# Kernel tuning notes

Measured on AMD Instinct MI355X. Metric: run time of the kernel, lower is better.

## Reference

```python
import jax, jax.numpy as jnp
import numpy as np

BANDLIMIT = 0.5
STEP_SCALE = 1.0  # refiner default step_scale_value
LN_EPS = 1e-5


def _layernorm(x, g, b):
    mu = jnp.mean(x, axis=-1, keepdims=True)
    xc = x - mu
    inv = jax.lax.rsqrt(jnp.mean(xc * xc, axis=-1, keepdims=True) + LN_EPS)
    return xc * inv * g + b


def setup_inputs() -> dict:
    key = jax.random.key(0)
    ks = jax.random.split(key, 12)
    B, C, H, W = 16, 384, 64, 64
    P = 192  # conj-sym half of state_dim=384
    x = jax.random.normal(ks[0], (B, C, H, W), dtype=jnp.float32)
    ln1_g = 1.0 + 0.1 * jax.random.normal(ks[1], (C,), dtype=jnp.float32)
    ln1_b = 0.1 * jax.random.normal(ks[2], (C,), dtype=jnp.float32)
    # stable diagonal A: negative real part, HiPPO-like imaginary ladder
    lam_re = -(0.3 + jax.random.uniform(ks[3], (P,), dtype=jnp.float32))
    lam_im = jnp.pi * jnp.arange(P, dtype=jnp.float32)
    Lambda = jnp.stack([lam_re, lam_im], axis=-1)          # [P,2] (re,im)
    Bmat = jax.random.normal(ks[4], (P, C, 2), dtype=jnp.float32) / np.sqrt(C)
    Cmat = jax.random.normal(ks[5], (C, P, 2), dtype=jnp.float32) / np.sqrt(P)
    D = jax.random.normal(ks[6], (C,), dtype=jnp.float32)
    log_step = jax.random.uniform(ks[7], (P,), dtype=jnp.float32,
                                  minval=float(np.log(1e-3)), maxval=float(np.log(0.1)))
    ln2_g = 1.0 + 0.1 * jax.random.normal(ks[8], (C,), dtype=jnp.float32)
    ln2_b = 0.1 * jax.random.normal(ks[9], (C,), dtype=jnp.float32)
    W_enc = jax.random.normal(ks[10], (2 * C, C), dtype=jnp.float32) / np.sqrt(C)
    W_dec = jax.random.normal(ks[11], (C, C), dtype=jnp.float32) / np.sqrt(C)
    return {"x": x, "ln1_g": ln1_g, "ln1_b": ln1_b, "Lambda": Lambda,
            "Bmat": Bmat, "Cmat": Cmat, "D": D, "log_step": log_step,
            "ln2_g": ln2_g, "ln2_b": ln2_b, "W_enc": W_enc, "W_dec": W_dec}


def reference(x, ln1_g, ln1_b, Lambda, Bmat, Cmat, D, log_step, ln2_g, ln2_b, W_enc, W_dec):
    Bsz, C, H, W = x.shape
    u = x.reshape(Bsz, C, H * W).transpose(0, 2, 1)        # [B, L, C]

    # --- S5Block: attn branch ---
    fx = _layernorm(u, ln1_g, ln1_b)
    res = fx

    lam = Lambda[..., 0] + 1j * Lambda[..., 1]             # [P] complex
    Bc = Bmat[..., 0] + 1j * Bmat[..., 1]                  # [P, C]
    Cc = Cmat[..., 0] + 1j * Cmat[..., 1]                  # [C, P]
    step = STEP_SCALE * jnp.exp(log_step)                  # [P]
    # bandlimit mask on C (as in S5 with bandlimit=0.5)
    freqs = (step / STEP_SCALE) * jnp.abs(Lambda[..., 1]) / (2.0 * jnp.pi)
    mask = (freqs < BANDLIMIT * 0.5).astype(Cc.dtype)
    Cc = Cc * mask
    # ZOH discretization
    lam_bar = jnp.exp(lam * step)                          # [P]
    B_bar = ((lam_bar - 1.0) / lam)[:, None] * Bc          # [P, C]
    Bu = jnp.einsum('ph,blh->blp', B_bar, fx.astype(B_bar.dtype))  # [B,L,P] complex
    lam_el = jnp.broadcast_to(lam_bar, Bu.shape)

    def binop(a, b):
        # linear recurrence composition: x <- a2*(a1*x + b1) + b2
        return a[0] * b[0], b[0] * a[1] + b[1]

    _, xs = jax.lax.associative_scan(binop, (lam_el, Bu), axis=1)  # [B,L,P]
    y = 2.0 * jnp.real(jnp.einsum('hp,blp->blh', Cc, xs)) + D * fx
    y = jax.nn.gelu(y, approximate=False) + res

    # --- S5Block: GEGLU FFN branch ---
    fy = _layernorm(y, ln2_g, ln2_b)
    z = fy @ W_enc.T                                       # [B,L,2C]
    z1, z2 = jnp.split(z, 2, axis=-1)
    z = z1 * jax.nn.gelu(z2, approximate=False)
    y = z @ W_dec.T + fy

    return y.transpose(0, 2, 1).reshape(Bsz, C, H, W)
```

## Files before the change

kernel.cpp:

```cpp
#include <hip/hip_runtime.h>
#include <hip/hip_bf16.h>
#include <math.h>

typedef __attribute__((ext_vector_type(4))) float f32x4;
typedef __attribute__((ext_vector_type(8))) short s16x8;
typedef unsigned short u16;
typedef unsigned int u32;

#define CDIM 384
#define PDIM 192
#define LDIM 4096
#define BSZ  16
#define MDIM 65536
#define KD   384
#define BM 128
#define BN 128
#define BK 32
#define NT (KD / BK)
#define BUFE (BM * BK)

__device__ __forceinline__ u16 f2bf(float f) {
    u32 x = __float_as_uint(f);
    x += 0x7fffu + ((x >> 16) & 1u);
    return (u16)(x >> 16);
}
__device__ __forceinline__ float bf2f(u16 v) {
    return __uint_as_float(((u32)v) << 16);
}
__device__ __forceinline__ float gelu_exact(float x) {
    return 0.5f * x * (1.0f + erff(x * 0.7071067811865476f));
}
__device__ __forceinline__ float gelu_fast(float x) {
    float w = -1.5957691216f * x * (1.0f + 0.044715f * x * x);
    return x / (1.0f + __expf(w));
}
__device__ __forceinline__ void gld_lds16(const u16* g, u16* l) {
    __builtin_amdgcn_global_load_lds(
        (const __attribute__((address_space(1))) void*)g,
        (__attribute__((address_space(3))) void*)l, 16, 0, 0);
}

__device__ __forceinline__ void swz_decode(int NY, int& mt, int& nt) {
    int bid = blockIdx.x + gridDim.x * blockIdx.y;
    int nwg = gridDim.x * gridDim.y;
    int cpx = nwg >> 3;
    int work = (bid & 7) * cpx + (bid >> 3);
    mt = work / NY;
    nt = work - mt * NY;
}

__global__ __launch_bounds__(256) void k_setup(
    const float* __restrict__ Lambda, const float* __restrict__ Bmat,
    const float* __restrict__ Cmat, const float* __restrict__ log_step,
    const float* __restrict__ W_enc, const float* __restrict__ W_dec,
    u16* __restrict__ Wb, u16* __restrict__ Wc, u16* __restrict__ We,
    u16* __restrict__ Wd, float* __restrict__ lam_bar)
{
    int idx = blockIdx.x * 256 + threadIdx.x;
    if (idx < 73728) {
        int p = idx / CDIM, c = idx % CDIM;
        float st  = expf(log_step[p]);
        float lre = Lambda[2*p], lim = Lambda[2*p+1];
        float el  = expf(lre * st);
        float lbr = el * cosf(lim * st);
        float lbi = el * sinf(lim * st);
        float dd  = lre*lre + lim*lim;
        float a = lbr - 1.0f, b = lbi;
        float cr = (a * lre + b * lim) / dd;
        float ci = (b * lre - a * lim) / dd;
        float Br = Bmat[2*(p*CDIM + c)], Bi = Bmat[2*(p*CDIM + c) + 1];
        Wb[p*KD + c]          = f2bf(cr*Br - ci*Bi);
        Wb[(PDIM + p)*KD + c] = f2bf(cr*Bi + ci*Br);
    } else if (idx < 147456) {
        int e = idx - 73728;
        int h = e / PDIM, p = e % PDIM;
        float st  = expf(log_step[p]);
        float lim = Lambda[2*p+1];
        float freq = st * fabsf(lim) / 6.283185307179586f;
        float sc = (freq < 0.25f) ? 2.0f : 0.0f;
        Wc[h*KD + p]        = f2bf( sc * Cmat[2*(h*PDIM + p)]);
        Wc[h*KD + PDIM + p] = f2bf(-sc * Cmat[2*(h*PDIM + p) + 1]);
    } else if (idx < 442368) {
        int e = idx - 147456;
        We[e] = f2bf(W_enc[e]);
    } else if (idx < 589824) {
        int e = idx - 442368;
        Wd[e] = f2bf(W_dec[e]);
    } else if (idx < 590016) {
        int p = idx - 589824;
        float st  = expf(log_step[p]);
        float lre = Lambda[2*p], lim = Lambda[2*p+1];
        float el  = expf(lre * st);
        lam_bar[2*p]   = el * cosf(lim * st);
        lam_bar[2*p+1] = el * sinf(lim * st);
    }
}

__global__ __launch_bounds__(256) void k_ln1(
    const float* __restrict__ x, const float* __restrict__ g,
    const float* __restrict__ bb, u16* __restrict__ fx)
{
    __shared__ float tile[CDIM * 36];
    __shared__ float mu_sh[32], inv_sh[32];
    int b  = blockIdx.x >> 7;
    int l0 = (blockIdx.x & 127) * 32;
    int tid = threadIdx.x;
    const float* src = x + ((size_t)b * CDIM) * LDIM + l0;
    #pragma unroll
    for (int it = 0; it < 12; it++) {
        int s = it * 256 + tid;
        int ch = s >> 3, c4 = (s & 7) * 4;
        float4 v = *(const float4*)(src + (size_t)ch * LDIM + c4);
        *(float4*)(tile + ch * 36 + c4) = v;
    }
    __syncthreads();
    int j = tid >> 3, k = tid & 7;
    float sum = 0.f, sq = 0.f;
    for (int c = k; c < CDIM; c += 8) {
        float v = tile[c * 36 + j];
        sum += v; sq += v * v;
    }
    sum += __shfl_xor(sum, 1); sq += __shfl_xor(sq, 1);
    sum += __shfl_xor(sum, 2); sq += __shfl_xor(sq, 2);
    sum += __shfl_xor(sum, 4); sq += __shfl_xor(sq, 4);
    float mu  = sum * (1.0f / CDIM);
    float var = sq * (1.0f / CDIM) - mu * mu;
    float inv = rsqrtf(var + 1e-5f);
    if (k == 0) { mu_sh[j] = mu; inv_sh[j] = inv; }
    __syncthreads();
    u16* dst = fx + ((size_t)(b * LDIM + l0)) * CDIM;
    #pragma unroll
    for (int it = 0; it < 12; it++) {
        int s  = it * 256 + tid;
        int cq = s % 96, jj = s / 96;
        int c  = cq * 4;
        float m2 = mu_sh[jj], iv = inv_sh[jj];
        float4 gv = *(const float4*)(g + c);
        float4 bv = *(const float4*)(bb + c);
        ushort4 o;
        o.x = f2bf((tile[(c+0)*36 + jj] - m2) * iv * gv.x + bv.x);
        o.y = f2bf((tile[(c+1)*36 + jj] - m2) * iv * gv.y + bv.y);
        o.z = f2bf((tile[(c+2)*36 + jj] - m2) * iv * gv.z + bv.z);
        o.w = f2bf((tile[(c+3)*36 + jj] - m2) * iv * gv.w + bv.w);
        *(ushort4*)(dst + (size_t)jj * CDIM + c) = o;
    }
}

template<bool SWAP>
__device__ __forceinline__ void gemm_core(
    const u16* __restrict__ A, int lda, const u16* __restrict__ Bw,
    int m0, int n0, u16* a_sh, u16* b_sh, f32x4 acc[4][4])
{
    const int tid  = threadIdx.x;
    const int w    = tid >> 6, lane = tid & 63;
    const int t16  = lane & 15, quad = lane >> 4;
    const int wm   = w >> 1,   wn   = w & 1;
    const int lr  = lane >> 2;
    const int cbg = (lane & 3) ^ ((lane >> 3) & 3);
    const u16* gA0 = A  + (size_t)(m0 + w*32 + lr) * lda + cbg*8;
    const u16* gA1 = gA0 + (size_t)16 * lda;
    const u16* gB0 = Bw + (size_t)(n0 + w*32 + lr) * KD + cbg*8;
    const u16* gB1 = gB0 + (size_t)16 * KD;
    u16* lA0 = a_sh + (w*32) * BK;
    u16* lA1 = lA0 + 16*BK;
    u16* lB0 = b_sh + (w*32) * BK;
    u16* lB1 = lB0 + 16*BK;
    const int pos = (quad ^ ((t16 >> 1) & 3)) * 8;
    const u16* ard = a_sh + (wm*64 + t16) * BK + pos;
    const u16* brd = b_sh + (wn*64 + t16) * BK + pos;
    #pragma unroll
    for (int i = 0; i < 4; i++)
        #pragma unroll
        for (int j = 0; j < 4; j++) acc[i][j] = (f32x4){0.f,0.f,0.f,0.f};
    gld_lds16(gA0, lA0);
    gld_lds16(gA1, lA1);
    gld_lds16(gB0, lB0);
    gld_lds16(gB1, lB1);
    gld_lds16(gA0 + BK, lA0 + BUFE);
    gld_lds16(gA1 + BK, lA1 + BUFE);
    gld_lds16(gB0 + BK, lB0 + BUFE);
    gld_lds16(gB1 + BK, lB1 + BUFE);
    #pragma unroll
    for (int t = 0; t < NT; ++t) {
        if (t < NT - 1) asm volatile("s_waitcnt vmcnt(4)" ::: "memory");
        else            asm volatile("s_waitcnt vmcnt(0)" ::: "memory");
        __builtin_amdgcn_s_barrier();
        __builtin_amdgcn_sched_barrier(0);
        if (t + 2 < NT) {
            const int kb = (t + 2) * BK;
            const int bo = ((t + 2) % 3) * BUFE;
            gld_lds16(gA0 + kb, lA0 + bo);
            gld_lds16(gA1 + kb, lA1 + bo);
            gld_lds16(gB0 + kb, lB0 + bo);
            gld_lds16(gB1 + kb, lB1 + bo);
        }
        __builtin_amdgcn_sched_barrier(0);
        const u16* ac = ard + (t % 3) * BUFE;
        const u16* bc = brd + (t % 3) * BUFE;
        s16x8 af[4], bfr[4];
        #pragma unroll
        for (int i = 0; i < 4; i++) af[i]  = *(const s16x8*)(ac + i*16*BK);
        #pragma unroll
        for (int j = 0; j < 4; j++) bfr[j] = *(const s16x8*)(bc + j*16*BK);
        #pragma unroll
        for (int i = 0; i < 4; i++)
            #pragma unroll
            for (int j = 0; j < 4; j++) {
                if (SWAP)
                    acc[i][j] = __builtin_amdgcn_mfma_f32_16x16x32_bf16(bfr[j], af[i], acc[i][j], 0,0,0);
                else
                    acc[i][j] = __builtin_amdgcn_mfma_f32_16x16x32_bf16(af[i], bfr[j], acc[i][j], 0,0,0);
            }
    }
}

__global__ __launch_bounds__(256) void k_gemm_bu(
    const u16* __restrict__ fx, const u16* __restrict__ Wb, u16* __restrict__ Bu)
{
    __shared__ __align__(16) u16 a_sh[3*BUFE], b_sh[3*BUFE];
    int mt, nt;
    swz_decode(gridDim.y, mt, nt);
    int m0 = mt * BM, n0 = nt * BN;
    f32x4 acc[4][4];
    gemm_core<false>(fx, CDIM, Wb, m0, n0, a_sh, b_sh, acc);
    int lane = threadIdx.x & 63, w = threadIdx.x >> 6;
    int t16 = lane & 15, quad = lane >> 4, wm = w >> 1, wn = w & 1;
    #pragma unroll
    for (int i = 0; i < 4; i++)
        #pragma unroll
        for (int j = 0; j < 4; j++)
            #pragma unroll
            for (int rr = 0; rr < 4; rr++) {
                int m = m0 + wm*64 + i*16 + quad*4 + rr;
                int n = n0 + wn*64 + j*16 + t16;
                Bu[(size_t)m * CDIM + n] = f2bf(acc[i][j][rr]);
            }
}

__global__ __launch_bounds__(256) void k_gemm_y(
    const u16* __restrict__ xs, const u16* __restrict__ Wc,
    const u16* __restrict__ fx, const float* __restrict__ Dv, u16* __restrict__ y)
{
    __shared__ __align__(16) u16 a_sh[3*BUFE], b_sh[3*BUFE];
    int mt, nt;
    swz_decode(gridDim.y, mt, nt);
    int m0 = mt * BM, n0 = nt * BN;
    f32x4 acc[4][4];
    gemm_core<false>(xs, CDIM, Wc, m0, n0, a_sh, b_sh, acc);
    int lane = threadIdx.x & 63, w = threadIdx.x >> 6;
    int t16 = lane & 15, quad = lane >> 4, wm = w >> 1, wn = w & 1;
    float dv[4];
    #pragma unroll
    for (int j = 0; j < 4; j++) dv[j] = Dv[n0 + wn*64 + j*16 + t16];
    #pragma unroll
    for (int i = 0; i < 4; i++)
        #pragma unroll
        for (int j = 0; j < 4; j++)
            #pragma unroll
            for (int rr = 0; rr < 4; rr++) {
                int m = m0 + wm*64 + i*16 + quad*4 + rr;
                int n = n0 + wn*64 + j*16 + t16;
                float fxv = bf2f(fx[(size_t)m * CDIM + n]);
                float v = acc[i][j][rr] + dv[j] * fxv;
                y[(size_t)m * CDIM + n] = f2bf(gelu_fast(v) + fxv);
            }
}

__global__ __launch_bounds__(256) void k_gemm_zg(
    const u16* __restrict__ fy, const u16* __restrict__ We, u16* __restrict__ zg)
{
    __shared__ __align__(16) u16 sh[6*BUFE];
    u16* a_sh = sh;
    u16* b_sh = sh + 3*BUFE;
    const int tid = threadIdx.x;
    const int w = tid >> 6, lane = tid & 63;
    const int t16 = lane & 15, quad = lane >> 4;
    const int wm = w >> 1, wn = w & 1;
    int mt, nt;
    swz_decode(gridDim.y, mt, nt);
    const int m0 = mt * BM;
    const int c0 = nt * 64;
    const int lr  = lane >> 2;
    const int cbg = (lane & 3) ^ ((lane >> 3) & 3);
    const u16* gA0 = fy + (size_t)(m0 + w*32 + lr) * CDIM + cbg*8;
    const u16* gA1 = gA0 + (size_t)16 * CDIM;
    int brow = c0 + w*32 + ((w >= 2) ? 320 : 0);
    const u16* gB0 = We + (size_t)(brow + lr) * KD + cbg*8;
    const u16* gB1 = gB0 + (size_t)16 * KD;
    u16* lA0 = a_sh + (w*32) * BK;
    u16* lA1 = lA0 + 16*BK;
    u16* lB0 = b_sh + (w*32) * BK;
    u16* lB1 = lB0 + 16*BK;
    const int pos = (quad ^ ((t16 >> 1) & 3)) * 8;
    const u16* ard = a_sh + (wm*64 + t16) * BK + pos;
    const u16* brd = b_sh + (wn*64 + t16) * BK + pos;
    f32x4 acc[4][4];
    #pragma unroll
    for (int i = 0; i < 4; i++)
        #pragma unroll
        for (int j = 0; j < 4; j++) acc[i][j] = (f32x4){0.f,0.f,0.f,0.f};
    gld_lds16(gA0, lA0);
    gld_lds16(gA1, lA1);
    gld_lds16(gB0, lB0);
    gld_lds16(gB1, lB1);
    gld_lds16(gA0 + BK, lA0 + BUFE);
    gld_lds16(gA1 + BK, lA1 + BUFE);
    gld_lds16(gB0 + BK, lB0 + BUFE);
    gld_lds16(gB1 + BK, lB1 + BUFE);
    #pragma unroll
    for (int t = 0; t < NT; ++t) {
        if (t < NT - 1) asm volatile("s_waitcnt vmcnt(4)" ::: "memory");
        else            asm volatile("s_waitcnt vmcnt(0)" ::: "memory");
        __builtin_amdgcn_s_barrier();
        __builtin_amdgcn_sched_barrier(0);
        if (t + 2 < NT) {
            const int kb = (t + 2) * BK;
            const int bo = ((t + 2) % 3) * BUFE;
            gld_lds16(gA0 + kb, lA0 + bo);
            gld_lds16(gA1 + kb, lA1 + bo);
            gld_lds16(gB0 + kb, lB0 + bo);
            gld_lds16(gB1 + kb, lB1 + bo);
        }
        __builtin_amdgcn_sched_barrier(0);
        const u16* ac = ard + (t % 3) * BUFE;
        const u16* bc = brd + (t % 3) * BUFE;
        s16x8 af[4], bfr[4];
        #pragma unroll
        for (int i = 0; i < 4; i++) af[i]  = *(const s16x8*)(ac + i*16*BK);
        #pragma unroll
        for (int j = 0; j < 4; j++) bfr[j] = *(const s16x8*)(brd ? (bc + j*16*BK) : nullptr);
        #pragma unroll
        for (int i = 0; i < 4; i++)
            #pragma unroll
            for (int j = 0; j < 4; j++)
                acc[i][j] = __builtin_amdgcn_mfma_f32_16x16x32_bf16(af[i], bfr[j], acc[i][j], 0,0,0);
    }
    __syncthreads();
    if (wn == 1) {
        #pragma unroll
        for (int i = 0; i < 4; i++)
            #pragma unroll
            for (int j = 0; j < 4; j++)
                #pragma unroll
                for (int rr = 0; rr < 4; rr++) {
                    int m = wm*64 + i*16 + quad*4 + rr;
                    int c = j*16 + t16;
                    sh[m*66 + c] = f2bf(gelu_fast(acc[i][j][rr]));
                }
    }
    __syncthreads();
    if (wn == 0) {
        #pragma unroll
        for (int i = 0; i < 4; i++)
            #pragma unroll
            for (int j = 0; j < 4; j++)
                #pragma unroll
                for (int rr = 0; rr < 4; rr++) {
                    int m = wm*64 + i*16 + quad*4 + rr;
                    int c = j*16 + t16;
                    float gv = bf2f(sh[m*66 + c]);
                    zg[(size_t)(m0 + m) * CDIM + c0 + c] = f2bf(acc[i][j][rr] * gv);
                }
    }
}

__global__ __launch_bounds__(256) void k_gemm_out(
    const u16* __restrict__ zg, const u16* __restrict__ Wd,
    const u16* __restrict__ fy, float* __restrict__ out)
{
    __shared__ __align__(16) u16 a_sh[3*BUFE], b_sh[3*BUFE];
    int mt, nt;
    swz_decode(gridDim.y, mt, nt);
    int m0 = mt * BM, n0 = nt * BN;
    f32x4 acc[4][4];
    gemm_core<true>(zg, CDIM, Wd, m0, n0, a_sh, b_sh, acc);
    int lane = threadIdx.x & 63, w = threadIdx.x >> 6;
    int t16 = lane & 15, quad = lane >> 4, wm = w >> 1, wn = w & 1;
    int b = m0 >> 12;
    #pragma unroll
    for (int i = 0; i < 4; i++)
        #pragma unroll
        for (int j = 0; j < 4; j++)
            #pragma unroll
            for (int rr = 0; rr < 4; rr++) {
                int nn = n0 + wn*64 + j*16 + quad*4 + rr;
                int mm = m0 + wm*64 + i*16 + t16;
                float fyv = bf2f(fy[(size_t)mm * CDIM + nn]);
                int l = mm & 4095;
                out[((size_t)(b * CDIM + nn)) * LDIM + l] = acc[i][j][rr] + fyv;
            }
}

__global__ __launch_bounds__(192) void k_scan_a(
    const u16* __restrict__ Bu, const float* __restrict__ lam_bar,
    float* __restrict__ summ)
{
    int b = blockIdx.x >> 6, ch = blockIdx.x & 63;
    int p = threadIdx.x;
    float lr = lam_bar[2*p], li = lam_bar[2*p+1];
    float xr = 0.f, xi = 0.f;
    const u16* base = Bu + (size_t)(b * LDIM + ch * 64) * CDIM;
    #pragma unroll 8
    for (int i = 0; i < 64; i++) {
        float br = bf2f(base[(size_t)i * CDIM + p]);
        float bi = bf2f(base[(size_t)i * CDIM + PDIM + p]);
        float nr = lr * xr - li * xi + br;
        float ni = lr * xi + li * xr + bi;
        xr = nr; xi = ni;
    }
    size_t o = (size_t)(b * 64 + ch) * CDIM + p;
    summ[o] = xr;
    summ[o + PDIM] = xi;
}

__global__ __launch_bounds__(256) void k_scan_b(
    const float* __restrict__ lam_bar, float* __restrict__ summ)
{
    int id = blockIdx.x * 256 + threadIdx.x;
    if (id >= BSZ * PDIM) return;
    int b = id / PDIM, p = id % PDIM;
    float ar = lam_bar[2*p], ai = lam_bar[2*p+1];
    #pragma unroll
    for (int s = 0; s < 6; s++) {
        float nr = ar * ar - ai * ai, ni = 2.f * ar * ai;
        ar = nr; ai = ni;
    }
    float cr = 0.f, ci = 0.f;
    #pragma unroll 4
    for (int ch = 0; ch < 64; ch++) {
        size_t o = (size_t)(b * 64 + ch) * CDIM + p;
        float sr = summ[o], si = summ[o + PDIM];
        summ[o] = cr; summ[o + PDIM] = ci;
        float nr = ar * cr - ai * ci + sr;
        float ni = ar * ci + ai * cr + si;
        cr = nr; ci = ni;
    }
}

__global__ __launch_bounds__(192) void k_scan_c(
    u16* __restrict__ Bu, const float* __restrict__ lam_bar,
    const float* __restrict__ summ)
{
    int b = blockIdx.x >> 6, ch = blockIdx.x & 63;
    int p = threadIdx.x;
    float lr = lam_bar[2*p], li = lam_bar[2*p+1];
    size_t oc = (size_t)(b * 64 + ch) * CDIM + p;
    float xr = summ[oc], xi = summ[oc + PDIM];
    u16* base = Bu + (size_t)(b * LDIM + ch * 64) * CDIM;
    #pragma unroll 8
    for (int i = 0; i < 64; i++) {
        float br = bf2f(base[(size_t)i * CDIM + p]);
        float bi = bf2f(base[(size_t)i * CDIM + PDIM + p]);
        float nr = lr * xr - li * xi + br;
        float ni = lr * xi + li * xr + bi;
        xr = nr; xi = ni;
        base[(size_t)i * CDIM + p] = f2bf(xr);
        base[(size_t)i * CDIM + PDIM + p] = f2bf(xi);
    }
}

__global__ __launch_bounds__(256) void k_ln2(
    const u16* __restrict__ y, const float* __restrict__ g,
    const float* __restrict__ bb, u16* __restrict__ fy)
{
    int w = threadIdx.x >> 6, lane = threadIdx.x & 63;
    size_t m = (size_t)blockIdx.x * 4 + w;
    const u16* row = y + m * CDIM;
    float v[6];
    float sum = 0.f, sq = 0.f;
    #pragma unroll
    for (int i = 0; i < 6; i++) {
        v[i] = bf2f(row[lane + 64 * i]);
        sum += v[i]; sq += v[i] * v[i];
    }
    #pragma unroll
    for (int o = 1; o < 64; o <<= 1) {
        sum += __shfl_xor(sum, o); sq += __shfl_xor(sq, o);
    }
    float mu  = sum * (1.0f / CDIM);
    float var = sq * (1.0f / CDIM) - mu * mu;
    float inv = rsqrtf(var + 1e-5f);
    u16* dst = fy + m * CDIM;
    #pragma unroll
    for (int i = 0; i < 6; i++) {
        int c = lane + 64 * i;
        dst[c] = f2bf((v[i] - mu) * inv * g[c] + bb[c]);
    }
}

extern "C" void kernel_launch(void* const* d_in, const int* in_sizes, int n_in,
                              void* d_out, int out_size, void* d_ws, size_t ws_size,
                              hipStream_t stream)
{
    const float* x        = (const float*)d_in[0];
    const float* ln1_g    = (const float*)d_in[1];
    const float* ln1_b    = (const float*)d_in[2];
    const float* Lambda   = (const float*)d_in[3];
    const float* Bmat     = (const float*)d_in[4];
    const float* Cmat     = (const float*)d_in[5];
    const float* Dvec     = (const float*)d_in[6];
    const float* log_step = (const float*)d_in[7];
    const float* ln2_g    = (const float*)d_in[8];
    const float* ln2_b    = (const float*)d_in[9];
    const float* W_enc    = (const float*)d_in[10];
    const float* W_dec    = (const float*)d_in[11];

    char* ws = (char*)d_ws;
    const size_t HBF = (size_t)MDIM * CDIM * 2;
    u16* fx = (u16*)(ws);
    u16* fy = (u16*)(ws + HBF);
    u16* bu = (u16*)(ws + 2 * HBF);
    u16* zg = (u16*)(ws + 2 * HBF);
    char* wbase = ws + 3 * HBF;
    u16* Wb = (u16*)(wbase);
    u16* Wc = (u16*)(wbase + 294912);
    u16* We = (u16*)(wbase + 589824);
    u16* Wd = (u16*)(wbase + 1179648);
    float* lam_bar = (float*)(wbase + 1474560);
    float* summ    = (float*)(wbase + 1476096);
    u16* yb  = (u16*)d_out;
    float* out = (float*)d_out;

    k_setup<<<2305, 256, 0, stream>>>(Lambda, Bmat, Cmat, log_step, W_enc, W_dec,
                                      Wb, Wc, We, Wd, lam_bar);
    k_ln1<<<2048, 256, 0, stream>>>(x, ln1_g, ln1_b, fx);
    k_gemm_bu<<<dim3(512, 3), 256, 0, stream>>>(fx, Wb, bu);
    k_scan_a<<<1024, 192, 0, stream>>>(bu, lam_bar, summ);
    k_scan_b<<<12, 256, 0, stream>>>(lam_bar, summ);
    k_scan_c<<<1024, 192, 0, stream>>>(bu, lam_bar, summ);
    k_gemm_y<<<dim3(512, 3), 256, 0, stream>>>(bu, Wc, fx, Dvec, yb);
    k_ln2<<<16384, 256, 0, stream>>>(yb, ln2_g, ln2_b, fy);
    k_gemm_zg<<<dim3(512, 6), 256, 0, stream>>>(fy, We, zg);
    k_gemm_out<<<dim3(512, 3), 256, 0, stream>>>(zg, Wd, fy, out);
}
```

Measured before the change: 428.0 us.

## Transpose LN1 shared tile to row-major and add MFMA priority hints in GEMMs

LN1 now stores the input tile transposed, token-major with padded stride 388, at staging time. The reduction and normalize passes can then read float4 vectors along channels instead of strided scalars, which should cut shared-memory read instructions and bank conflicts; the cost is four scalar LDS stores per element during staging. Both GEMM main loops also raise wave priority around the MFMA block with s_setprio, add an explicit lgkmcnt wait plus a sched barrier, and drop an odd null-pointer select on the B fragment load. These scheduling hints may help interleave waves across the MFMA and load phases, or they may serialize them.

```diff
diff --git a/kernel.cpp b/kernel.cpp
--- a/kernel.cpp
+++ b/kernel.cpp
@@ -96,11 +96,12 @@
     }
 }
 
+#define LNS 388
 __global__ __launch_bounds__(256) void k_ln1(
     const float* __restrict__ x, const float* __restrict__ g,
     const float* __restrict__ bb, u16* __restrict__ fx)
 {
-    __shared__ float tile[CDIM * 36];
+    __shared__ float tile[32 * LNS];
     __shared__ float mu_sh[32], inv_sh[32];
     int b  = blockIdx.x >> 7;
     int l0 = (blockIdx.x & 127) * 32;
@@ -109,16 +110,22 @@
     #pragma unroll
     for (int it = 0; it < 12; it++) {
         int s = it * 256 + tid;
-        int ch = s >> 3, c4 = (s & 7) * 4;
-        float4 v = *(const float4*)(src + (size_t)ch * LDIM + c4);
-        *(float4*)(tile + ch * 36 + c4) = v;
+        int ch = s >> 3, k4 = s & 7;
+        float4 v = *(const float4*)(src + (size_t)ch * LDIM + k4 * 4);
+        float* t0 = tile + (k4 * 4) * LNS + ch;
+        t0[0]       = v.x;
+        t0[LNS]     = v.y;
+        t0[2*LNS]   = v.z;
+        t0[3*LNS]   = v.w;
     }
     __syncthreads();
     int j = tid >> 3, k = tid & 7;
     float sum = 0.f, sq = 0.f;
-    for (int c = k; c < CDIM; c += 8) {
-        float v = tile[c * 36 + j];
-        sum += v; sq += v * v;
+    #pragma unroll
+    for (int m = 0; m < 12; m++) {
+        float4 v = *(const float4*)(tile + j * LNS + (k + 8*m) * 4);
+        sum += v.x + v.y + v.z + v.w;
+        sq  += v.x*v.x + v.y*v.y + v.z*v.z + v.w*v.w;
     }
     sum += __shfl_xor(sum, 1); sq += __shfl_xor(sq, 1);
     sum += __shfl_xor(sum, 2); sq += __shfl_xor(sq, 2);
@@ -137,11 +144,12 @@
         float m2 = mu_sh[jj], iv = inv_sh[jj];
         float4 gv = *(const float4*)(g + c);
         float4 bv = *(const float4*)(bb + c);
+        float4 v  = *(const float4*)(tile + jj * LNS + c);
         ushort4 o;
-        o.x = f2bf((tile[(c+0)*36 + jj] - m2) * iv * gv.x + bv.x);
-        o.y = f2bf((tile[(c+1)*36 + jj] - m2) * iv * gv.y + bv.y);
-        o.z = f2bf((tile[(c+2)*36 + jj] - m2) * iv * gv.z + bv.z);
-        o.w = f2bf((tile[(c+3)*36 + jj] - m2) * iv * gv.w + bv.w);
+        o.x = f2bf((v.x - m2) * iv * gv.x + bv.x);
+        o.y = f2bf((v.y - m2) * iv * gv.y + bv.y);
+        o.z = f2bf((v.z - m2) * iv * gv.z + bv.z);
+        o.w = f2bf((v.w - m2) * iv * gv.w + bv.w);
         *(ushort4*)(dst + (size_t)jj * CDIM + c) = o;
     }
 }
@@ -202,6 +210,7 @@
         for (int i = 0; i < 4; i++) af[i]  = *(const s16x8*)(ac + i*16*BK);
         #pragma unroll
         for (int j = 0; j < 4; j++) bfr[j] = *(const s16x8*)(bc + j*16*BK);
+        __builtin_amdgcn_s_setprio(1);
         #pragma unroll
         for (int i = 0; i < 4; i++)
             #pragma unroll
@@ -211,6 +220,9 @@
                 else
                     acc[i][j] = __builtin_amdgcn_mfma_f32_16x16x32_bf16(af[i], bfr[j], acc[i][j], 0,0,0);
             }
+        __builtin_amdgcn_s_setprio(0);
+        asm volatile("s_waitcnt lgkmcnt(0)" ::: "memory");
+        __builtin_amdgcn_sched_barrier(0);
     }
 }
 
@@ -328,12 +340,16 @@
         #pragma unroll
         for (int i = 0; i < 4; i++) af[i]  = *(const s16x8*)(ac + i*16*BK);
         #pragma unroll
-        for (int j = 0; j < 4; j++) bfr[j] = *(const s16x8*)(brd ? (bc + j*16*BK) : nullptr);
+        for (int j = 0; j < 4; j++) bfr[j] = *(const s16x8*)(bc + j*16*BK);
+        __builtin_amdgcn_s_setprio(1);
         #pragma unroll
         for (int i = 0; i < 4; i++)
             #pragma unroll
             for (int j = 0; j < 4; j++)
                 acc[i][j] = __builtin_amdgcn_mfma_f32_16x16x32_bf16(af[i], bfr[j], acc[i][j], 0,0,0);
+        __builtin_amdgcn_s_setprio(0);
+        asm volatile("s_waitcnt lgkmcnt(0)" ::: "memory");
+        __builtin_amdgcn_sched_barrier(0);
     }
     __syncthreads();
     if (wn == 1) {
```

Result: no change. 423.0 us (-1.2%).
